# Optimization experiments

Measured on AMD Instinct MI355X. Metric: run time of the kernel, lower is better.

Reference implementation:

```python
import jax, jax.numpy as jnp
import numpy as np
import math

B, S, E, H = 4, 1024, 768, 12
HD = E // H

def setup_inputs() -> dict:
    key = jax.random.key(0)
    ks = jax.random.split(key, 13)
    inp = {
        'query': jax.random.normal(ks[0], (B, S, E), jnp.float32),
        'key':   jax.random.normal(ks[1], (B, S, E), jnp.float32),
        'value': jax.random.normal(ks[2], (B, S, E), jnp.float32),
        'mask':  jax.random.randint(ks[3], (B, S, S), 0, 2, jnp.int32),
    }
    scale = 1.0 / math.sqrt(E)
    for i, nm in enumerate(['q', 'k', 'v', 'o']):
        inp[f'W{nm}'] = jax.random.normal(ks[4 + 2 * i], (E, E), jnp.float32) * scale
        inp[f'b{nm}'] = jax.random.normal(ks[5 + 2 * i], (E,), jnp.float32) * 0.01
    return inp


def reference(query, key, value, mask, Wq, bq, Wk, bk, Wv, bv, Wo, bo):
    # QKV projections (torch Linear: x @ W.T + b), split into heads -> [B,H,S,HD]
    def proj(x, W, b):
        y = x @ W.T + b
        return y.reshape(B, S, H, HD).transpose(0, 2, 1, 3)

    q = proj(query, Wq, bq)
    k = proj(key, Wk, bk)
    v = proj(value, Wv, bv)

    scores = jnp.einsum('bhqd,bhkd->bhqk', q, k) / jnp.sqrt(jnp.float32(HD))
    m = mask[:, None, :, :]  # [B,1,S,S] broadcast over heads
    # multiply-then-masked_fill semantics of the original module
    scores = scores * m.astype(scores.dtype)
    scores = jnp.where(m == 0, -jnp.inf, scores)
    attn = jax.nn.softmax(scores, axis=-1)
    # nan_to_num for fully-masked rows (all -inf -> NaN -> 0)
    attn = jnp.where(jnp.isnan(attn), 0.0, attn)
    # dropout omitted (eval/deterministic reference)
    xv = jnp.einsum('bhqk,bhkd->bhqd', attn, v)
    xv = xv.transpose(0, 2, 1, 3).reshape(B, S, E)
    out = xv @ Wo.T + bo
    return out
```

## Files before the change

kernel.cpp:

```cpp
#include <hip/hip_runtime.h>

typedef __bf16 bf16x8 __attribute__((ext_vector_type(8)));
typedef float floatx4 __attribute__((ext_vector_type(4)));

#define B_ 4
#define S_ 1024
#define E_ 768
#define H_ 12
#define HD_ 64

__device__ __forceinline__ void async16(const void* g, void* l) {
  __builtin_amdgcn_global_load_lds((const __attribute__((address_space(1))) void*)g,
                                   (__attribute__((address_space(3))) void*)l, 16, 0, 0);
}

__device__ __forceinline__ floatx4 mfma16(bf16x8 a, bf16x8 b, floatx4 c) {
  return __builtin_amdgcn_mfma_f32_16x16x32_bf16(a, b, c, 0, 0, 0);
}

__global__ __launch_bounds__(256) void prep_kernel(
    const float* __restrict__ q, const float* __restrict__ k, const float* __restrict__ v,
    const float* __restrict__ w0, const float* __restrict__ w1,
    const float* __restrict__ w2, const float* __restrict__ w3,
    const int* __restrict__ mask,
    __bf16* __restrict__ xin, __bf16* __restrict__ wb,
    unsigned long long* __restrict__ bm) {
  const int bx = blockIdx.x;
  if (bx < 4608) {
    const int z = bx / 1536, xb = bx % 1536;
    const float* s = (z == 0) ? q : (z == 1) ? k : v;
    __bf16* d = xin + (size_t)z * (size_t)(B_ * S_ * E_);
    const size_t i8 = (size_t)xb * 256 + threadIdx.x;
    const float4* sp = (const float4*)s + i8 * 2;
    float4 a = sp[0], bb = sp[1];
    bf16x8 o;
    o[0] = (__bf16)a.x; o[1] = (__bf16)a.y; o[2] = (__bf16)a.z; o[3] = (__bf16)a.w;
    o[4] = (__bf16)bb.x; o[5] = (__bf16)bb.y; o[6] = (__bf16)bb.z; o[7] = (__bf16)bb.w;
    *(bf16x8*)(d + i8 * 8) = o;
  } else if (bx < 5760) {
    const int t = bx - 4608;
    const int z = t / 288, xb = t % 288;
    const float* s = (z == 0) ? w0 : (z == 1) ? w1 : (z == 2) ? w2 : w3;
    __bf16* d = wb + (size_t)z * (size_t)(E_ * E_);
    const size_t i8 = (size_t)xb * 256 + threadIdx.x;
    const float4* sp = (const float4*)s + i8 * 2;
    float4 a = sp[0], bb = sp[1];
    bf16x8 o;
    o[0] = (__bf16)a.x; o[1] = (__bf16)a.y; o[2] = (__bf16)a.z; o[3] = (__bf16)a.w;
    o[4] = (__bf16)bb.x; o[5] = (__bf16)bb.y; o[6] = (__bf16)bb.z; o[7] = (__bf16)bb.w;
    *(bf16x8*)(d + i8 * 8) = o;
  } else {
    const int row = bx - 5760;
    const int wave = threadIdx.x >> 6, lane = threadIdx.x & 63;
#pragma unroll
    for (int pass = 0; pass < 4; ++pass) {
      const int kk = pass * 256 + wave * 64 + lane;
      const int mv = mask[(size_t)row * S_ + kk];
      const unsigned long long bal = __ballot(mv != 0);
      if (lane == 0) bm[(size_t)row * 16 + pass * 4 + wave] = bal;
    }
  }
}

__global__ __launch_bounds__(256, 3) void proj_qkv_kernel(
    const __bf16* __restrict__ Xq, const __bf16* __restrict__ Xk, const __bf16* __restrict__ Xv,
    const __bf16* __restrict__ Wq, const __bf16* __restrict__ Wk, const __bf16* __restrict__ Wv,
    const float* __restrict__ bq, const float* __restrict__ bk, const float* __restrict__ bv,
    __bf16* __restrict__ Qf, __bf16* __restrict__ Kf, __bf16* __restrict__ Vt) {
  const int z = blockIdx.z;
  const __bf16* X = (z == 0) ? Xq : (z == 1) ? Xk : Xv;
  const __bf16* W = (z == 0) ? Wq : (z == 1) ? Wk : Wv;
  const float* bias = (z == 0) ? bq : (z == 1) ? bk : bv;

  const int tid = threadIdx.x;
  const int wave = tid >> 6, lane = tid & 63;
  const int l15 = lane & 15, quad = lane >> 4;
  const int wr = wave >> 1, wc = wave & 1;
  const int bm = blockIdx.y * 128, bn = blockIdx.x * 128;
  const int srl = lane >> 3, sch = lane & 7;

  __shared__ alignas(16) unsigned char smem[4 * 64 * 72 * 2];
  __bf16* As = (__bf16*)smem;
  __bf16* Bs = (__bf16*)(smem + 16384);
  __bf16* ST = (__bf16*)smem + (size_t)wave * (64 * 72);

  floatx4 zf = {0.0f, 0.0f, 0.0f, 0.0f};
  floatx4 acc[4][4];
#pragma unroll
  for (int i = 0; i < 4; ++i)
#pragma unroll
    for (int j = 0; j < 4; ++j) acc[i][j] = zf;

  for (int kk = 0; kk < E_; kk += 64) {
#pragma unroll
    for (int c = 0; c < 4; ++c) {
      const int s = c * 4 + wave;
      const int row = s * 8 + srl;
      const int xo = (sch ^ (row & 7)) * 8;
      async16(X + (size_t)(bm + row) * E_ + kk + xo, &As[s * 512]);
      async16(W + (size_t)(bn + row) * E_ + kk + xo, &Bs[s * 512]);
    }
    __syncthreads();
#pragma unroll
    for (int ks = 0; ks < 2; ++ks) {
      bf16x8 af[4], bfr[4];
#pragma unroll
      for (int i = 0; i < 4; ++i) {
        const int m = wr * 64 + i * 16 + l15;
        af[i] = *(const bf16x8*)&As[m * 64 + (((ks * 4 + quad) ^ (m & 7)) * 8)];
      }
#pragma unroll
      for (int j = 0; j < 4; ++j) {
        const int n = wc * 64 + j * 16 + l15;
        bfr[j] = *(const bf16x8*)&Bs[n * 64 + (((ks * 4 + quad) ^ (n & 7)) * 8)];
      }
#pragma unroll
      for (int i = 0; i < 4; ++i)
#pragma unroll
        for (int j = 0; j < 4; ++j)
          acc[i][j] = mfma16(af[i], bfr[j], acc[i][j]);
    }
    __syncthreads();
  }

  if (z < 2) {
    __bf16* dst = (z == 0) ? Qf : Kf;
    const float sc = (z == 0) ? 0.125f : 1.0f;
#pragma unroll
    for (int j = 0; j < 4; ++j) {
      const float bval = bias[bn + wc * 64 + j * 16 + l15];
#pragma unroll
      for (int i = 0; i < 4; ++i)
#pragma unroll
        for (int r = 0; r < 4; ++r)
          ST[(i * 16 + quad * 4 + r) * 72 + j * 16 + l15] =
              (__bf16)((acc[i][j][r] + bval) * sc);
    }
#pragma unroll
    for (int t = 0; t < 8; ++t) {
      const int row = t * 8 + (lane >> 3), ch = lane & 7;
      bf16x8 vrow = *(const bf16x8*)&ST[row * 72 + ch * 8];
      *(bf16x8*)&dst[(size_t)(bm + wr * 64 + row) * E_ + bn + wc * 64 + ch * 8] = vrow;
    }
  } else {
#pragma unroll
    for (int j = 0; j < 4; ++j) {
      const float bval = bias[bn + wc * 64 + j * 16 + l15];
#pragma unroll
      for (int i = 0; i < 4; ++i)
#pragma unroll
        for (int r = 0; r < 4; ++r)
          ST[(j * 16 + l15) * 72 + i * 16 + quad * 4 + r] = (__bf16)(acc[i][j][r] + bval);
    }
    const int hh = (bn + wc * 64) >> 6;
    const int m0 = bm + wr * 64;
    const int bb = m0 >> 10, ss0 = m0 & 1023;
#pragma unroll
    for (int t = 0; t < 8; ++t) {
      const int d = t * 8 + (lane >> 3), ch = lane & 7;
      bf16x8 vrow = *(const bf16x8*)&ST[d * 72 + ch * 8];
      *(bf16x8*)&Vt[(((size_t)bb * H_ + hh) * HD_ + d) * S_ + ss0 + ch * 8] = vrow;
    }
  }
}

__global__ __launch_bounds__(256, 4) void proj_out_kernel(
    const __bf16* __restrict__ X, const __bf16* __restrict__ W,
    const float* __restrict__ bias, float* __restrict__ out) {
  const int tid = threadIdx.x;
  const int wave = tid >> 6, lane = tid & 63;
  const int l15 = lane & 15, quad = lane >> 4;
  const int wr = wave >> 1, wc = wave & 1;
  const int bm = blockIdx.y * 64, bn = blockIdx.x * 64;
  const int srl = lane >> 3, sch = lane & 7;

  __shared__ alignas(16) __bf16 As[64 * 64];
  __shared__ alignas(16) __bf16 Bs[64 * 64];

  floatx4 zf = {0.0f, 0.0f, 0.0f, 0.0f};
  floatx4 acc[2][2];
#pragma unroll
  for (int i = 0; i < 2; ++i)
#pragma unroll
    for (int j = 0; j < 2; ++j) acc[i][j] = zf;

  for (int kk = 0; kk < E_; kk += 64) {
#pragma unroll
    for (int c = 0; c < 2; ++c) {
      const int s = c * 4 + wave;
      const int row = s * 8 + srl;
      const int xo = (sch ^ (row & 7)) * 8;
      async16(X + (size_t)(bm + row) * E_ + kk + xo, &As[s * 512]);
      async16(W + (size_t)(bn + row) * E_ + kk + xo, &Bs[s * 512]);
    }
    __syncthreads();
#pragma unroll
    for (int ks = 0; ks < 2; ++ks) {
      bf16x8 af[2], bfr[2];
#pragma unroll
      for (int i = 0; i < 2; ++i) {
        const int m = wr * 32 + i * 16 + l15;
        af[i] = *(const bf16x8*)&As[m * 64 + (((ks * 4 + quad) ^ (m & 7)) * 8)];
      }
#pragma unroll
      for (int j = 0; j < 2; ++j) {
        const int n = wc * 32 + j * 16 + l15;
        bfr[j] = *(const bf16x8*)&Bs[n * 64 + (((ks * 4 + quad) ^ (n & 7)) * 8)];
      }
#pragma unroll
      for (int i = 0; i < 2; ++i)
#pragma unroll
        for (int j = 0; j < 2; ++j)
          acc[i][j] = mfma16(af[i], bfr[j], acc[i][j]);
    }
    __syncthreads();
  }

#pragma unroll
  for (int j = 0; j < 2; ++j) {
    const int n = bn + wc * 32 + j * 16 + l15;
    const float bval = bias[n];
#pragma unroll
    for (int i = 0; i < 2; ++i) {
#pragma unroll
      for (int r = 0; r < 4; ++r) {
        const int m = bm + wr * 32 + i * 16 + quad * 4 + r;
        out[(size_t)m * E_ + n] = acc[i][j][r] + bval;
      }
    }
  }
}

#define MSHIFT 12.0f
#define PSTR 72
__global__ __launch_bounds__(256, 3) void attn_kernel(
    const __bf16* __restrict__ Qf, const __bf16* __restrict__ Kf,
    const __bf16* __restrict__ Vt, const unsigned long long* __restrict__ bmask,
    __bf16* __restrict__ XV) {
  const int tid = threadIdx.x;
  const int wave = tid >> 6, lane = tid & 63;
  const int l15 = lane & 15, quad = lane >> 4;
  const int bh = blockIdx.x;
  const int b = bh / H_, h = bh % H_;
  const int q0 = blockIdx.y * 64 + wave * 16;

  __shared__ alignas(16) __bf16 Kbuf[2][64 * 64];
  __shared__ alignas(16) __bf16 Vbuf[2][64 * 64];
  __shared__ alignas(16) __bf16 Ps[4 * 16 * PSTR];
  __bf16* Pw = &Ps[wave * 16 * PSTR];

  const __bf16* qb = Qf + ((size_t)b * S_ + q0) * E_ + h * HD_;
  bf16x8 af[2];
  af[0] = *(const bf16x8*)(qb + (size_t)l15 * E_ + quad * 8);
  af[1] = *(const bf16x8*)(qb + (size_t)l15 * E_ + 32 + quad * 8);

  const __bf16* kbase = Kf + (size_t)b * S_ * E_ + h * HD_;
  const __bf16* vbase = Vt + (size_t)bh * HD_ * S_;
  const unsigned long long* mbm = bmask + ((size_t)b * S_ + q0) * 16;

  const int srow = tid >> 3, sch = tid & 7;
#pragma unroll
  for (int c = 0; c < 2; ++c) {
    const int row = c * 32 + srow;
    const int xo = (sch ^ (row & 7)) * 8;
    async16(kbase + (size_t)row * E_ + xo, &Kbuf[0][(c * 256 + tid) * 8]);
    async16(vbase + (size_t)row * S_ + xo, &Vbuf[0][(c * 256 + tid) * 8]);
  }

  floatx4 zf = {0.0f, 0.0f, 0.0f, 0.0f};
  floatx4 o[4];
  float lrow[4];
#pragma unroll
  for (int jd = 0; jd < 4; ++jd) o[jd] = zf;
#pragma unroll
  for (int r = 0; r < 4; ++r) lrow[r] = 0.0f;

  for (int kt = 0; kt < 16; ++kt) {
    const int p = kt & 1;
    const int k0 = kt * 64;
    __syncthreads();

    if (kt < 15) {
      const int kn = k0 + 64;
#pragma unroll
      for (int c = 0; c < 2; ++c) {
        const int row = c * 32 + srow;
        const int xo = (sch ^ (row & 7)) * 8;
        async16(kbase + (size_t)(kn + row) * E_ + xo, &Kbuf[1 - p][(c * 256 + tid) * 8]);
        async16(vbase + (size_t)row * S_ + kn + xo, &Vbuf[1 - p][(c * 256 + tid) * 8]);
      }
    }

    unsigned long long bmsh[4];
#pragma unroll
    for (int r = 0; r < 4; ++r)
      bmsh[r] = mbm[(size_t)(quad * 4 + r) * 16 + kt] >> l15;

    bf16x8 bk[4][2];
#pragma unroll
    for (int j = 0; j < 4; ++j) {
      const int key = j * 16 + l15;
#pragma unroll
      for (int ks = 0; ks < 2; ++ks)
        bk[j][ks] = *(const bf16x8*)&Kbuf[p][key * 64 + ((ks * 4 + quad) ^ (key & 7)) * 8];
    }
    bf16x8 bvf[4][2];
#pragma unroll
    for (int jd = 0; jd < 4; ++jd) {
      const int d = jd * 16 + l15;
#pragma unroll
      for (int ks2 = 0; ks2 < 2; ++ks2)
        bvf[jd][ks2] = *(const bf16x8*)&Vbuf[p][d * 64 + ((ks2 * 4 + quad) ^ (d & 7)) * 8];
    }

    floatx4 sc[4];
#pragma unroll
    for (int j = 0; j < 4; ++j) sc[j] = zf;
#pragma unroll
    for (int j = 0; j < 4; ++j) {
      sc[j] = mfma16(af[0], bk[j][0], sc[j]);
      sc[j] = mfma16(af[1], bk[j][1], sc[j]);
    }

#pragma unroll
    for (int j = 0; j < 4; ++j)
#pragma unroll
      for (int r = 0; r < 4; ++r) {
        float pv = __expf(sc[j][r] - MSHIFT);
        pv = ((bmsh[r] >> (j * 16)) & 1ull) ? pv : 0.0f;
        lrow[r] += pv;
        Pw[(quad * 4 + r) * PSTR + j * 16 + l15] = (__bf16)pv;
      }

#pragma unroll
    for (int ks2 = 0; ks2 < 2; ++ks2) {
      bf16x8 pa = *(const bf16x8*)&Pw[l15 * PSTR + ks2 * 32 + quad * 8];
#pragma unroll
      for (int jd = 0; jd < 4; ++jd) o[jd] = mfma16(pa, bvf[jd][ks2], o[jd]);
    }
  }

#pragma unroll
  for (int sh = 1; sh < 16; sh <<= 1)
#pragma unroll
    for (int r = 0; r < 4; ++r) lrow[r] += __shfl_xor(lrow[r], sh, 64);
  float linv[4];
#pragma unroll
  for (int r = 0; r < 4; ++r) linv[r] = (lrow[r] > 0.0f) ? (1.0f / lrow[r]) : 0.0f;
  __bf16* xbase = XV + ((size_t)b * S_ + q0) * E_ + h * HD_;
#pragma unroll
  for (int jd = 0; jd < 4; ++jd)
#pragma unroll
    for (int r = 0; r < 4; ++r)
      xbase[(size_t)(quad * 4 + r) * E_ + jd * 16 + l15] = (__bf16)(o[jd][r] * linv[r]);
}

extern "C" void kernel_launch(void* const* d_in, const int* in_sizes, int n_in,
                              void* d_out, int out_size, void* d_ws, size_t ws_size,
                              hipStream_t stream) {
  const float* query = (const float*)d_in[0];
  const float* key   = (const float*)d_in[1];
  const float* value = (const float*)d_in[2];
  const int*   mask  = (const int*)d_in[3];
  const float* Wq = (const float*)d_in[4];
  const float* bq = (const float*)d_in[5];
  const float* Wk = (const float*)d_in[6];
  const float* bk = (const float*)d_in[7];
  const float* Wv = (const float*)d_in[8];
  const float* bv = (const float*)d_in[9];
  const float* Wo = (const float*)d_in[10];
  const float* bo = (const float*)d_in[11];
  float* out = (float*)d_out;

  const size_t NX = (size_t)B_ * S_ * E_;
  const size_t NW = (size_t)E_ * E_;
  __bf16* ws = (__bf16*)d_ws;
  __bf16* xq  = ws;
  __bf16* xk  = xq + NX;
  __bf16* xv  = xk + NX;
  __bf16* wqb = xv + NX;
  __bf16* wkb = wqb + NW;
  __bf16* wvb = wkb + NW;
  __bf16* wob = wvb + NW;
  __bf16* Qf  = wob + NW;
  __bf16* Kf  = Qf + NX;
  __bf16* Vt  = Kf + NX;
  __bf16* XVb = Vt + NX;
  unsigned long long* bmask = (unsigned long long*)(XVb + NX);

  prep_kernel<<<dim3(9856), 256, 0, stream>>>(query, key, value, Wq, Wk, Wv, Wo,
                                              mask, xq, wqb, bmask);
  proj_qkv_kernel<<<dim3(6, 32, 3), 256, 0, stream>>>(xq, xk, xv, wqb, wkb, wvb,
                                                      bq, bk, bv, Qf, Kf, Vt);
  attn_kernel<<<dim3(48, 16), 256, 0, stream>>>(Qf, Kf, Vt, bmask, XVb);
  proj_out_kernel<<<dim3(12, 64), 256, 0, stream>>>(XVb, wob, bo, out);
}
```

Before: 189.4 us.

## Double-buffer projection GEMM tiles, swap grid order, prefetch mask bits in attention

Both projection GEMM kernels now double-buffer their LDS tiles. The next K-slice is issued asynchronously while the current one is multiplied, and the trailing barrier per iteration is removed. Grid axes are swapped so consecutive blocks walk the M dimension and share weight tiles in cache. The attention kernel software-prefetches the next tile's mask bitmask words. The cost is doubled LDS use (64KB for proj_qkv, lowering its occupancy bound to 2) and a little more register pressure.

```diff
diff --git a/kernel.cpp b/kernel.cpp
--- a/kernel.cpp
+++ b/kernel.cpp
@@ -62,7 +62,7 @@
   }
 }
 
-__global__ __launch_bounds__(256, 3) void proj_qkv_kernel(
+__global__ __launch_bounds__(256, 2) void proj_qkv_kernel(
     const __bf16* __restrict__ Xq, const __bf16* __restrict__ Xk, const __bf16* __restrict__ Xv,
     const __bf16* __restrict__ Wq, const __bf16* __restrict__ Wk, const __bf16* __restrict__ Wv,
     const float* __restrict__ bq, const float* __restrict__ bk, const float* __restrict__ bv,
@@ -76,12 +76,10 @@
   const int wave = tid >> 6, lane = tid & 63;
   const int l15 = lane & 15, quad = lane >> 4;
   const int wr = wave >> 1, wc = wave & 1;
-  const int bm = blockIdx.y * 128, bn = blockIdx.x * 128;
+  const int bm = blockIdx.x * 128, bn = blockIdx.y * 128;
   const int srl = lane >> 3, sch = lane & 7;
 
-  __shared__ alignas(16) unsigned char smem[4 * 64 * 72 * 2];
-  __bf16* As = (__bf16*)smem;
-  __bf16* Bs = (__bf16*)(smem + 16384);
+  __shared__ alignas(16) unsigned char smem[65536];
   __bf16* ST = (__bf16*)smem + (size_t)wave * (64 * 72);
 
   floatx4 zf = {0.0f, 0.0f, 0.0f, 0.0f};
@@ -91,16 +89,35 @@
 #pragma unroll
     for (int j = 0; j < 4; ++j) acc[i][j] = zf;
 
-  for (int kk = 0; kk < E_; kk += 64) {
-#pragma unroll
-    for (int c = 0; c < 4; ++c) {
-      const int s = c * 4 + wave;
-      const int row = s * 8 + srl;
-      const int xo = (sch ^ (row & 7)) * 8;
-      async16(X + (size_t)(bm + row) * E_ + kk + xo, &As[s * 512]);
-      async16(W + (size_t)(bn + row) * E_ + kk + xo, &Bs[s * 512]);
-    }
+#pragma unroll
+  for (int c = 0; c < 4; ++c) {
+    const int s = c * 4 + wave;
+    const int row = s * 8 + srl;
+    const int xo = (sch ^ (row & 7)) * 8;
+    async16(X + (size_t)(bm + row) * E_ + xo, (__bf16*)smem + s * 512);
+    async16(W + (size_t)(bn + row) * E_ + xo, (__bf16*)(smem + 16384) + s * 512);
+  }
+
+  for (int kt = 0; kt < 12; ++kt) {
+    const int p = kt & 1;
+    __bf16* As = (__bf16*)(smem + p * 32768);
+    __bf16* Bs = (__bf16*)(smem + p * 32768 + 16384);
     __syncthreads();
+
+    if (kt < 11) {
+      const int kk = (kt + 1) * 64;
+      __bf16* An = (__bf16*)(smem + (1 - p) * 32768);
+      __bf16* Bn = (__bf16*)(smem + (1 - p) * 32768 + 16384);
+#pragma unroll
+      for (int c = 0; c < 4; ++c) {
+        const int s = c * 4 + wave;
+        const int row = s * 8 + srl;
+        const int xo = (sch ^ (row & 7)) * 8;
+        async16(X + (size_t)(bm + row) * E_ + kk + xo, An + s * 512);
+        async16(W + (size_t)(bn + row) * E_ + kk + xo, Bn + s * 512);
+      }
+    }
+
 #pragma unroll
     for (int ks = 0; ks < 2; ++ks) {
       bf16x8 af[4], bfr[4];
@@ -120,8 +137,8 @@
         for (int j = 0; j < 4; ++j)
           acc[i][j] = mfma16(af[i], bfr[j], acc[i][j]);
     }
-    __syncthreads();
-  }
+  }
+  __syncthreads();
 
   if (z < 2) {
     __bf16* dst = (z == 0) ? Qf : Kf;
@@ -171,11 +188,10 @@
   const int wave = tid >> 6, lane = tid & 63;
   const int l15 = lane & 15, quad = lane >> 4;
   const int wr = wave >> 1, wc = wave & 1;
-  const int bm = blockIdx.y * 64, bn = blockIdx.x * 64;
+  const int bm = blockIdx.x * 64, bn = blockIdx.y * 64;
   const int srl = lane >> 3, sch = lane & 7;
 
-  __shared__ alignas(16) __bf16 As[64 * 64];
-  __shared__ alignas(16) __bf16 Bs[64 * 64];
+  __shared__ alignas(16) unsigned char smem[32768];
 
   floatx4 zf = {0.0f, 0.0f, 0.0f, 0.0f};
   floatx4 acc[2][2];
@@ -184,16 +200,35 @@
 #pragma unroll
     for (int j = 0; j < 2; ++j) acc[i][j] = zf;
 
-  for (int kk = 0; kk < E_; kk += 64) {
-#pragma unroll
-    for (int c = 0; c < 2; ++c) {
-      const int s = c * 4 + wave;
-      const int row = s * 8 + srl;
-      const int xo = (sch ^ (row & 7)) * 8;
-      async16(X + (size_t)(bm + row) * E_ + kk + xo, &As[s * 512]);
-      async16(W + (size_t)(bn + row) * E_ + kk + xo, &Bs[s * 512]);
-    }
+#pragma unroll
+  for (int c = 0; c < 2; ++c) {
+    const int s = c * 4 + wave;
+    const int row = s * 8 + srl;
+    const int xo = (sch ^ (row & 7)) * 8;
+    async16(X + (size_t)(bm + row) * E_ + xo, (__bf16*)smem + s * 512);
+    async16(W + (size_t)(bn + row) * E_ + xo, (__bf16*)(smem + 8192) + s * 512);
+  }
+
+  for (int kt = 0; kt < 12; ++kt) {
+    const int p = kt & 1;
+    __bf16* As = (__bf16*)(smem + p * 16384);
+    __bf16* Bs = (__bf16*)(smem + p * 16384 + 8192);
     __syncthreads();
+
+    if (kt < 11) {
+      const int kk = (kt + 1) * 64;
+      __bf16* An = (__bf16*)(smem + (1 - p) * 16384);
+      __bf16* Bn = (__bf16*)(smem + (1 - p) * 16384 + 8192);
+#pragma unroll
+      for (int c = 0; c < 2; ++c) {
+        const int s = c * 4 + wave;
+        const int row = s * 8 + srl;
+        const int xo = (sch ^ (row & 7)) * 8;
+        async16(X + (size_t)(bm + row) * E_ + kk + xo, An + s * 512);
+        async16(W + (size_t)(bn + row) * E_ + kk + xo, Bn + s * 512);
+      }
+    }
+
 #pragma unroll
     for (int ks = 0; ks < 2; ++ks) {
       bf16x8 af[2], bfr[2];
@@ -213,7 +248,6 @@
         for (int j = 0; j < 2; ++j)
           acc[i][j] = mfma16(af[i], bfr[j], acc[i][j]);
     }
-    __syncthreads();
   }
 
 #pragma unroll
@@ -267,6 +301,11 @@
     async16(vbase + (size_t)row * S_ + xo, &Vbuf[0][(c * 256 + tid) * 8]);
   }
 
+  unsigned long long bmsh[4];
+#pragma unroll
+  for (int r = 0; r < 4; ++r)
+    bmsh[r] = mbm[(size_t)(quad * 4 + r) * 16 + 0] >> l15;
+
   floatx4 zf = {0.0f, 0.0f, 0.0f, 0.0f};
   floatx4 o[4];
   float lrow[4];
@@ -291,10 +330,12 @@
       }
     }
 
-    unsigned long long bmsh[4];
-#pragma unroll
-    for (int r = 0; r < 4; ++r)
-      bmsh[r] = mbm[(size_t)(quad * 4 + r) * 16 + kt] >> l15;
+    unsigned long long bmnext[4];
+    if (kt < 15) {
+#pragma unroll
+      for (int r = 0; r < 4; ++r)
+        bmnext[r] = mbm[(size_t)(quad * 4 + r) * 16 + kt + 1] >> l15;
+    }
 
     bf16x8 bk[4][2];
 #pragma unroll
@@ -337,6 +378,11 @@
       bf16x8 pa = *(const bf16x8*)&Pw[l15 * PSTR + ks2 * 32 + quad * 8];
 #pragma unroll
       for (int jd = 0; jd < 4; ++jd) o[jd] = mfma16(pa, bvf[jd][ks2], o[jd]);
+    }
+
+    if (kt < 15) {
+#pragma unroll
+      for (int r = 0; r < 4; ++r) bmsh[r] = bmnext[r];
     }
   }
 
@@ -390,8 +436,8 @@
 
   prep_kernel<<<dim3(9856), 256, 0, stream>>>(query, key, value, Wq, Wk, Wv, Wo,
                                               mask, xq, wqb, bmask);
-  proj_qkv_kernel<<<dim3(6, 32, 3), 256, 0, stream>>>(xq, xk, xv, wqb, wkb, wvb,
+  proj_qkv_kernel<<<dim3(32, 6, 3), 256, 0, stream>>>(xq, xk, xv, wqb, wkb, wvb,
                                                       bq, bk, bv, Qf, Kf, Vt);
   attn_kernel<<<dim3(48, 16), 256, 0, stream>>>(Qf, Kf, Vt, bmask, XVb);
-  proj_out_kernel<<<dim3(12, 64), 256, 0, stream>>>(XVb, wob, bo, out);
-}
+  proj_out_kernel<<<dim3(64, 12), 256, 0, stream>>>(XVb, wob, bo, out);
+}
```

After: 183.1 us. 1.03x faster.
